# Kernel optimization log

Hardware: AMD Instinct MI355X
Metric: run time of the kernel (lower is better)

Reference implementation:

```python
import jax, jax.numpy as jnp
import numpy as np

N_HEAD = 16
NEG_INF = -1e9


def setup_inputs() -> dict:
    key = jax.random.key(0)
    k1, k2, k3 = jax.random.split(key, 3)
    B, S, D = 4, 1024, 1024
    x = jax.random.normal(k1, (B, S, D), dtype=jnp.float32)
    w_attn = jax.random.normal(k2, (D, 3 * D), dtype=jnp.float32) * 0.02
    b_attn = jnp.zeros((3 * D,), dtype=jnp.float32)
    w_proj = jax.random.normal(k3, (D, D), dtype=jnp.float32) * 0.02
    b_proj = jnp.zeros((D,), dtype=jnp.float32)
    return {"x": x, "w_attn": w_attn, "b_attn": b_attn,
            "w_proj": w_proj, "b_proj": b_proj}


def reference(x, w_attn, b_attn, w_proj, b_proj):
    B, S, D = x.shape
    H = N_HEAD
    hd = D // H
    # fused QKV Conv1D: addmm over flattened tokens
    qkv = x @ w_attn + b_attn                      # [B,S,3D]
    q, k, v = jnp.split(qkv, 3, axis=-1)           # each [B,S,D]
    # split heads -> [B,H,S,hd]
    def heads(t):
        return t.reshape(B, S, H, hd).transpose(0, 2, 1, 3)
    q, k, v = heads(q), heads(k), heads(v)
    # scaled dot-product with causal mask
    scores = jnp.einsum('bhqd,bhkd->bhqk', q, k) / jnp.sqrt(jnp.float32(hd))
    causal = jnp.tril(jnp.ones((S, S), dtype=bool))[None, None]  # [1,1,S,S]
    scores = jnp.where(causal, scores, NEG_INF)
    attn = jax.nn.softmax(scores, axis=-1)
    out = jnp.einsum('bhqk,bhkd->bhqd', attn, v)   # [B,H,S,hd]
    out = out.transpose(0, 2, 1, 3).reshape(B, S, D)  # merge heads
    # output projection Conv1D
    return out @ w_proj + b_proj
```

## Files before the change

### kernel.cpp

```cpp
#include <hip/hip_runtime.h>
#include <hip/hip_bf16.h>

typedef __attribute__((ext_vector_type(8))) __bf16 bf16x8;
typedef __attribute__((ext_vector_type(4))) float f32x4;

__device__ __forceinline__ unsigned short f2bf(float f) {
  unsigned int u = __builtin_bit_cast(unsigned int, f);
  u += 0x7fffu + ((u >> 16) & 1u);
  return (unsigned short)(u >> 16);
}

__device__ __forceinline__ unsigned int cvtpk_bf16(float a, float b) {
  unsigned int r;
  asm("v_cvt_pk_bf16_f32 %0, %1, %2" : "=v"(r) : "v"(a), "v"(b));
  return r;
}

__device__ __forceinline__ void gll16(const void* g, void* l) {
  __builtin_amdgcn_global_load_lds(
      (const __attribute__((address_space(1))) void*)g,
      (__attribute__((address_space(3))) void*)l, 16, 0, 0);
}

__device__ __forceinline__ bf16x8 lds_frag(const unsigned short* base, int row, int kbyte) {
  int off = row * 128 + (kbyte ^ ((row & 7) << 4));
  return *(const bf16x8*)((const char*)base + off);
}

__global__ __launch_bounds__(256) void prep(
    const float* __restrict__ x, unsigned short* __restrict__ xb,
    const float* __restrict__ wa, unsigned short* __restrict__ waT,
    const float* __restrict__ wp, unsigned short* __restrict__ wpT) {
  __shared__ float tile[32][33];
  const int b = blockIdx.x;
  const int t = threadIdx.x;
  if (b < 4096) {
    int i = (b * 256 + t) * 4;
    float4 v = *(const float4*)(x + i);
    ushort4 o;
    o.x = f2bf(v.x); o.y = f2bf(v.y); o.z = f2bf(v.z); o.w = f2bf(v.w);
    *(ushort4*)(xb + i) = o;
    return;
  }
  const float* in;
  unsigned short* out;
  int bid, N;
  if (b < 7168) { in = wa; out = waT; bid = b - 4096; N = 3072; }
  else          { in = wp; out = wpT; bid = b - 7168; N = 1024; }
  const int K = 1024;
  int nb = N >> 5;
  int bx = bid % nb, by = bid / nb;
  int n0 = bx << 5, k0 = by << 5;
  int c = t & 31, r0 = t >> 5;
#pragma unroll
  for (int i = 0; i < 4; ++i) {
    int r = r0 + i * 8;
    tile[r][c] = in[(size_t)(k0 + r) * N + n0 + c];
  }
  __syncthreads();
#pragma unroll
  for (int i = 0; i < 4; ++i) {
    int r = r0 + i * 8;
    out[(size_t)(n0 + r) * K + k0 + c] = f2bf(tile[c][r]);
  }
}

__global__ __launch_bounds__(512, 2) void gemm_qkv256(
    const unsigned short* __restrict__ A, const unsigned short* __restrict__ Bt,
    const float* __restrict__ bias,
    unsigned short* __restrict__ Qg, unsigned short* __restrict__ Kg,
    unsigned short* __restrict__ Vtg, int K) {
  __shared__ __align__(16) unsigned short SMEM[65536];
  unsigned short* const A0 = SMEM;
  unsigned short* const B0 = SMEM + 16384;
  unsigned short* const A1 = SMEM + 32768;
  unsigned short* const B1 = SMEM + 49152;
  const int t = threadIdx.x;
  const int l = t & 63, lr = l & 15, hi = l >> 4;
  const int w = t >> 6;
  const int wr = w >> 2, wc = w & 3;
  const int bid = (int)(blockIdx.x % 8) * 24 + (int)(blockIdx.x / 8);
  const int bm = bid / 12, bn = bid % 12;
  const int m0 = bm << 8, n0 = bn << 8;
  const int wbase = (t & ~63) * 8;

  f32x4 acc[8][4] = {};

  auto stage = [&](int kt, unsigned short* Ad, unsigned short* Bd) {
    const unsigned short* Ab = A + (size_t)m0 * K + kt * 64;
    const unsigned short* Bb = Bt + (size_t)n0 * K + kt * 64;
#pragma unroll
    for (int i = 0; i < 4; ++i) {
      int ci = i * 512 + t;
      int row = ci >> 3, cpos = ci & 7;
      int c = cpos ^ (row & 7);
      gll16(Ab + (size_t)row * K + c * 8, Ad + i * 4096 + wbase);
      gll16(Bb + (size_t)row * K + c * 8, Bd + i * 4096 + wbase);
    }
  };

  auto compute = [&](const unsigned short* Ad, const unsigned short* Bd) {
#pragma unroll
    for (int ks = 0; ks < 2; ++ks) {
      bf16x8 af[8], bv[4];
#pragma unroll
      for (int mi = 0; mi < 8; ++mi)
        af[mi] = lds_frag(Ad, wr * 128 + mi * 16 + lr, ks * 64 + hi * 16);
#pragma unroll
      for (int ni = 0; ni < 4; ++ni)
        bv[ni] = lds_frag(Bd, wc * 64 + ni * 16 + lr, ks * 64 + hi * 16);
      __builtin_amdgcn_s_setprio(1);
#pragma unroll
      for (int mi = 0; mi < 8; ++mi)
#pragma unroll
        for (int ni = 0; ni < 4; ++ni)
          acc[mi][ni] = __builtin_amdgcn_mfma_f32_16x16x32_bf16(af[mi], bv[ni], acc[mi][ni], 0, 0, 0);
      __builtin_amdgcn_s_setprio(0);
    }
  };

  const int nt = K >> 6;
  stage(0, A0, B0);
  __syncthreads();
  for (int T = 0; T < nt; ++T) {
    if (T + 1 < nt) stage(T + 1, (T & 1) ? A0 : A1, (T & 1) ? B0 : B1);
    compute((T & 1) ? A1 : A0, (T & 1) ? B1 : B0);
    __syncthreads();
  }

  if (n0 < 2048) {
    const float QSCALE = 0.125f * 1.4426950408889634f;
#pragma unroll
    for (int mi = 0; mi < 8; ++mi)
#pragma unroll
      for (int ni = 0; ni < 4; ++ni)
#pragma unroll
        for (int r = 0; r < 4; ++r) {
          int m = m0 + wr * 128 + mi * 16 + 4 * hi + r;
          int n = n0 + wc * 64 + ni * 16 + lr;
          float v = acc[mi][ni][r] + bias[n];
          int b = m >> 10, s = m & 1023;
          int d = n & 1023;
          int h = d >> 6, di = d & 63;
          int bh = (b << 4) + h;
          if (n < 1024) Qg[((size_t)(bh << 10) + s) * 64 + di] = f2bf(v * QSCALE);
          else          Kg[((size_t)(bh << 10) + s) * 64 + di] = f2bf(v);
        }
  } else {
    __syncthreads();
#pragma unroll
    for (int mi = 0; mi < 8; ++mi)
#pragma unroll
      for (int ni = 0; ni < 4; ++ni) {
        int nl = wc * 64 + ni * 16 + lr;
        int ml = wr * 128 + mi * 16 + 4 * hi;
        ushort4 pk;
        pk.x = f2bf(acc[mi][ni][0] + bias[n0 + nl]);
        pk.y = f2bf(acc[mi][ni][1] + bias[n0 + nl]);
        pk.z = f2bf(acc[mi][ni][2] + bias[n0 + nl]);
        pk.w = f2bf(acc[mi][ni][3] + bias[n0 + nl]);
        *(ushort4*)&SMEM[nl * 256 + (ml ^ ((nl & 7) << 3))] = pk;
      }
    __syncthreads();
    const int b = m0 >> 10;
    const int sbase = m0 & 1023;
#pragma unroll
    for (int it = 0; it < 16; ++it) {
      int nl = it * 16 + (t >> 5);
      int s0 = (t & 31) * 8;
      bf16x8 v8 = *(const bf16x8*)&SMEM[nl * 256 + (s0 ^ ((nl & 7) << 3))];
      int d = n0 - 2048 + nl;
      size_t row = ((size_t)((b << 4) + (d >> 6)) << 6) + (d & 63);
      *(bf16x8*)&Vtg[row * 1024 + sbase + s0] = v8;
    }
  }
}

__global__ __launch_bounds__(256, 2) void gemm_proj128(
    const unsigned short* __restrict__ A, const unsigned short* __restrict__ Bt,
    const float* __restrict__ bias, float* __restrict__ outf,
    int M, int N, int K) {
  __shared__ unsigned short A0[128 * 64], B0[128 * 64];
  __shared__ unsigned short A1[128 * 64], B1[128 * 64];
  const int t = threadIdx.x;
  const int w = t >> 6, l = t & 63, lr = l & 15, hi = l >> 4;
  const int wr = w >> 1, wc = w & 1;
  const int nbn = N >> 7;
  const int nwg = (M >> 7) * nbn;
  int bid = (int)blockIdx.x;
  if ((nwg & 7) == 0) bid = (bid % 8) * (nwg / 8) + bid / 8;
  const int bm = bid / nbn, bn = bid % nbn;
  const int m0 = bm << 7, n0 = bn << 7;
  const int wbase = (t & ~63) * 8;

  f32x4 acc[4][4] = {};

  auto stage = [&](int kt, unsigned short* Ad, unsigned short* Bd) {
    const unsigned short* Ab = A + (size_t)m0 * K + kt * 64;
    const unsigned short* Bb = Bt + (size_t)n0 * K + kt * 64;
#pragma unroll
    for (int i = 0; i < 4; ++i) {
      int ci = i * 256 + t;
      int row = ci >> 3, cpos = ci & 7;
      int c = cpos ^ (row & 7);
      gll16(Ab + (size_t)row * K + c * 8, Ad + i * 2048 + wbase);
      gll16(Bb + (size_t)row * K + c * 8, Bd + i * 2048 + wbase);
    }
  };

  auto compute = [&](const unsigned short* Ad, const unsigned short* Bd) {
#pragma unroll
    for (int ks = 0; ks < 2; ++ks) {
      bf16x8 af[4], bv[4];
#pragma unroll
      for (int mi = 0; mi < 4; ++mi)
        af[mi] = lds_frag(Ad, wr * 64 + mi * 16 + lr, ks * 64 + hi * 16);
#pragma unroll
      for (int ni = 0; ni < 4; ++ni)
        bv[ni] = lds_frag(Bd, wc * 64 + ni * 16 + lr, ks * 64 + hi * 16);
      __builtin_amdgcn_s_setprio(1);
#pragma unroll
      for (int mi = 0; mi < 4; ++mi)
#pragma unroll
        for (int ni = 0; ni < 4; ++ni)
          acc[mi][ni] = __builtin_amdgcn_mfma_f32_16x16x32_bf16(af[mi], bv[ni], acc[mi][ni], 0, 0, 0);
      __builtin_amdgcn_s_setprio(0);
    }
  };

  const int nt = K >> 6;
  stage(0, A0, B0);
  __syncthreads();
  for (int T = 0; T < nt; ++T) {
    if (T + 1 < nt) stage(T + 1, (T & 1) ? A0 : A1, (T & 1) ? B0 : B1);
    compute((T & 1) ? A1 : A0, (T & 1) ? B1 : B0);
    __syncthreads();
  }

#pragma unroll
  for (int mi = 0; mi < 4; ++mi)
#pragma unroll
    for (int ni = 0; ni < 4; ++ni)
#pragma unroll
      for (int r = 0; r < 4; ++r) {
        int m = m0 + wr * 64 + mi * 16 + 4 * hi + r;
        int n = n0 + wc * 64 + ni * 16 + lr;
        outf[(size_t)m * N + n] = acc[mi][ni][r] + bias[n];
      }
}

__global__ __launch_bounds__(256) void attn_kernel(
    const unsigned short* __restrict__ Qg, const unsigned short* __restrict__ Kg,
    const unsigned short* __restrict__ Vtg, unsigned short* __restrict__ Og) {
  __shared__ unsigned short K0[64 * 64], K1[64 * 64];
  __shared__ unsigned short Vb[64 * 64];
  __shared__ __align__(16) unsigned short Plds[4][16][72];
  const int bh = blockIdx.x & 63;
  const int qt = blockIdx.x >> 6;
  const int t = threadIdx.x;
  const int w = t >> 6, l = t & 63, lr = l & 15, hi = l >> 4;
  const unsigned short* Qbh = Qg + (size_t)bh * 65536;
  const unsigned short* Kbh = Kg + (size_t)bh * 65536;
  const unsigned short* Vbh = Vtg + (size_t)bh * 65536;
  const int q0 = qt * 64 + w * 16;
  const int wbase = (t & ~63) * 8;

  bf16x8 qf[2];
#pragma unroll
  for (int ks = 0; ks < 2; ++ks)
    qf[ks] = *(const bf16x8*)(Qbh + (size_t)(q0 + lr) * 64 + ks * 32 + hi * 8);

  f32x4 ocT[4] = {};
  float mrun = -1e30f, lrun = 0.f;
  const int thr = w * 16 + lr - 4 * hi;

  auto stageK = [&](int kt, unsigned short* Kd) {
#pragma unroll
    for (int i = 0; i < 2; ++i) {
      int ci = i * 256 + t;
      int row = ci >> 3, cpos = ci & 7;
      int c = cpos ^ (row & 7);
      gll16(Kbh + (size_t)(kt * 64 + row) * 64 + c * 8, Kd + i * 2048 + wbase);
    }
  };
  auto stageV = [&](int kt) {
#pragma unroll
    for (int i = 0; i < 2; ++i) {
      int ci = i * 256 + t;
      int row = ci >> 3, cpos = ci & 7;
      int c = cpos ^ (row & 7);
      gll16(Vbh + (size_t)row * 1024 + kt * 64 + c * 8, Vb + i * 2048 + wbase);
    }
  };

  stageK(0, K0);
  stageV(0);

  for (int kt = 0; kt <= qt; ++kt) {
    unsigned short* Kc = (kt & 1) ? K1 : K0;
    unsigned short* Kn = (kt & 1) ? K0 : K1;
    const bool pf = (kt < qt);

    asm volatile("s_waitcnt vmcnt(2)" ::: "memory");
    __builtin_amdgcn_s_barrier();

    if (pf) stageK(kt + 1, Kn);

    f32x4 sc[4] = {};
    __builtin_amdgcn_s_setprio(1);
#pragma unroll
    for (int c = 0; c < 4; ++c)
#pragma unroll
      for (int ks = 0; ks < 2; ++ks) {
        bf16x8 kf = lds_frag(Kc, c * 16 + lr, ks * 64 + hi * 16);
        sc[c] = __builtin_amdgcn_mfma_f32_16x16x32_bf16(kf, qf[ks], sc[c], 0, 0, 0);
      }
    __builtin_amdgcn_s_setprio(0);
    if (kt == qt) {
#pragma unroll
      for (int c = 0; c < 4; ++c)
#pragma unroll
        for (int r = 0; r < 4; ++r)
          if (c * 16 + r > thr) sc[c][r] = -1e30f;
    }

    float mx = sc[0][0];
#pragma unroll
    for (int c = 0; c < 4; ++c)
#pragma unroll
      for (int r = 0; r < 4; ++r) mx = fmaxf(mx, sc[c][r]);
    mx = fmaxf(mx, __shfl_xor(mx, 16));
    mx = fmaxf(mx, __shfl_xor(mx, 32));
    if (!__all(mx <= mrun)) {
      float mn = fmaxf(mrun, mx);
      float al = exp2f(mrun - mn);
      mrun = mn;
      lrun *= al;
#pragma unroll
      for (int c = 0; c < 4; ++c)
#pragma unroll
        for (int r = 0; r < 4; ++r) ocT[c][r] *= al;
    }
    float p[4][4], s = 0.f;
#pragma unroll
    for (int c = 0; c < 4; ++c)
#pragma unroll
      for (int r = 0; r < 4; ++r) {
        p[c][r] = exp2f(sc[c][r] - mrun);
        s += p[c][r];
      }
    s += __shfl_xor(s, 16);
    s += __shfl_xor(s, 32);
    lrun += s;

#pragma unroll
    for (int c = 0; c < 4; ++c) {
      uint2 pk;
      pk.x = cvtpk_bf16(p[c][0], p[c][1]);
      pk.y = cvtpk_bf16(p[c][2], p[c][3]);
      *(uint2*)&Plds[w][lr][c * 16 + 4 * hi] = pk;
    }
    asm volatile("s_waitcnt lgkmcnt(0)" ::: "memory");
    __builtin_amdgcn_sched_barrier(0);

    bf16x8 pb[2];
#pragma unroll
    for (int ks = 0; ks < 2; ++ks)
      pb[ks] = *(const bf16x8*)(&Plds[w][lr][ks * 32 + hi * 8]);

    if (pf) asm volatile("s_waitcnt vmcnt(2)" ::: "memory");
    else    asm volatile("s_waitcnt vmcnt(0)" ::: "memory");
    __builtin_amdgcn_s_barrier();

    __builtin_amdgcn_s_setprio(1);
#pragma unroll
    for (int c = 0; c < 4; ++c)
#pragma unroll
      for (int ks = 0; ks < 2; ++ks) {
        bf16x8 vf = lds_frag(Vb, c * 16 + lr, ks * 64 + hi * 16);
        ocT[c] = __builtin_amdgcn_mfma_f32_16x16x32_bf16(vf, pb[ks], ocT[c], 0, 0, 0);
      }
    __builtin_amdgcn_s_setprio(0);
    __builtin_amdgcn_s_barrier();
    if (pf) stageV(kt + 1);
  }

  const int b = bh >> 4, h = bh & 15;
  const float inv = 1.0f / lrun;
  const size_t rowbase = ((size_t)(b * 1024 + q0 + lr)) * 1024 + h * 64;
#pragma unroll
  for (int c = 0; c < 4; ++c) {
    uint2 o2;
    o2.x = cvtpk_bf16(ocT[c][0] * inv, ocT[c][1] * inv);
    o2.y = cvtpk_bf16(ocT[c][2] * inv, ocT[c][3] * inv);
    *(uint2*)&Og[rowbase + c * 16 + 4 * hi] = o2;
  }
}

extern "C" void kernel_launch(void* const* d_in, const int* in_sizes, int n_in,
                              void* d_out, int out_size, void* d_ws, size_t ws_size,
                              hipStream_t stream) {
  const float* x      = (const float*)d_in[0];
  const float* w_attn = (const float*)d_in[1];
  const float* b_attn = (const float*)d_in[2];
  const float* w_proj = (const float*)d_in[3];
  const float* b_proj = (const float*)d_in[4];
  float* out = (float*)d_out;

  unsigned short* ws  = (unsigned short*)d_ws;
  unsigned short* xb  = ws;
  unsigned short* waT = xb + 4096 * 1024;
  unsigned short* wpT = waT + 3072 * 1024;
  unsigned short* Qg  = wpT + 1024 * 1024;
  unsigned short* Kg  = Qg + 4194304;
  unsigned short* Vtg = Kg + 4194304;
  unsigned short* Og  = xb;

  prep<<<8192, 256, 0, stream>>>(x, xb, w_attn, waT, w_proj, wpT);
  gemm_qkv256<<<16 * 12, 512, 0, stream>>>(xb, waT, b_attn, Qg, Kg, Vtg, 1024);
  attn_kernel<<<1024, 256, 0, stream>>>(Qg, Kg, Vtg, Og);
  gemm_proj128<<<32 * 8, 256, 0, stream>>>(Og, wpT, b_proj, (float*)out, 4096, 1024, 1024);
}
```

Before: 97.59 us.

## Fuse x fp32-to-bf16 conversion into QKV GEMM A-tile loading

Removes the separate pass in prep that converts x to bf16. The QKV GEMM now reads fp32 x directly into registers, converts it to bf16 with packed cvt instructions, and writes it into the swizzled LDS tile after the compute step, keeping the double-buffer prefetch. This saves a full write and re-read of the 8 MB bf16 copy of x. In exchange, each GEMM block reads A as fp32 (twice the bytes, repeated across the 12 N-blocks), uses more registers for the prefetch, and loses the asynchronous global-to-LDS path for A.

Result: slower. 107.6 us (+10.3%).

```diff
diff --git a/kernel.cpp b/kernel.cpp
--- a/kernel.cpp
+++ b/kernel.cpp
@@ -28,25 +28,16 @@
 }
 
 __global__ __launch_bounds__(256) void prep(
-    const float* __restrict__ x, unsigned short* __restrict__ xb,
     const float* __restrict__ wa, unsigned short* __restrict__ waT,
     const float* __restrict__ wp, unsigned short* __restrict__ wpT) {
   __shared__ float tile[32][33];
   const int b = blockIdx.x;
   const int t = threadIdx.x;
-  if (b < 4096) {
-    int i = (b * 256 + t) * 4;
-    float4 v = *(const float4*)(x + i);
-    ushort4 o;
-    o.x = f2bf(v.x); o.y = f2bf(v.y); o.z = f2bf(v.z); o.w = f2bf(v.w);
-    *(ushort4*)(xb + i) = o;
-    return;
-  }
   const float* in;
   unsigned short* out;
   int bid, N;
-  if (b < 7168) { in = wa; out = waT; bid = b - 4096; N = 3072; }
-  else          { in = wp; out = wpT; bid = b - 7168; N = 1024; }
+  if (b < 3072) { in = wa; out = waT; bid = b; N = 3072; }
+  else          { in = wp; out = wpT; bid = b - 3072; N = 1024; }
   const int K = 1024;
   int nb = N >> 5;
   int bx = bid % nb, by = bid / nb;
@@ -66,7 +57,7 @@
 }
 
 __global__ __launch_bounds__(512, 2) void gemm_qkv256(
-    const unsigned short* __restrict__ A, const unsigned short* __restrict__ Bt,
+    const float* __restrict__ Xf, const unsigned short* __restrict__ Bt,
     const float* __restrict__ bias,
     unsigned short* __restrict__ Qg, unsigned short* __restrict__ Kg,
     unsigned short* __restrict__ Vtg, int K) {
@@ -85,16 +76,43 @@
   const int wbase = (t & ~63) * 8;
 
   f32x4 acc[8][4] = {};
-
-  auto stage = [&](int kt, unsigned short* Ad, unsigned short* Bd) {
-    const unsigned short* Ab = A + (size_t)m0 * K + kt * 64;
+  float4 fa[4][2];
+
+  size_t Aoff[4];
+#pragma unroll
+  for (int i = 0; i < 4; ++i) {
+    int ci = i * 512 + t;
+    int row = ci >> 3, cpos = ci & 7;
+    int c = cpos ^ (row & 7);
+    Aoff[i] = (size_t)(m0 + row) * 1024 + c * 8;
+  }
+
+  auto loadA = [&](int kt) {
+#pragma unroll
+    for (int i = 0; i < 4; ++i) {
+      const float* src = Xf + Aoff[i] + kt * 64;
+      fa[i][0] = *(const float4*)(src);
+      fa[i][1] = *(const float4*)(src + 4);
+    }
+  };
+  auto writeA = [&](unsigned short* Ad) {
+#pragma unroll
+    for (int i = 0; i < 4; ++i) {
+      uint4 pk;
+      pk.x = cvtpk_bf16(fa[i][0].x, fa[i][0].y);
+      pk.y = cvtpk_bf16(fa[i][0].z, fa[i][0].w);
+      pk.z = cvtpk_bf16(fa[i][1].x, fa[i][1].y);
+      pk.w = cvtpk_bf16(fa[i][1].z, fa[i][1].w);
+      *(uint4*)&Ad[(size_t)(i * 512 + t) * 8] = pk;
+    }
+  };
+  auto stageB = [&](int kt, unsigned short* Bd) {
     const unsigned short* Bb = Bt + (size_t)n0 * K + kt * 64;
 #pragma unroll
     for (int i = 0; i < 4; ++i) {
       int ci = i * 512 + t;
       int row = ci >> 3, cpos = ci & 7;
       int c = cpos ^ (row & 7);
-      gll16(Ab + (size_t)row * K + c * 8, Ad + i * 4096 + wbase);
       gll16(Bb + (size_t)row * K + c * 8, Bd + i * 4096 + wbase);
     }
   };
@@ -120,11 +138,17 @@
   };
 
   const int nt = K >> 6;
-  stage(0, A0, B0);
+  loadA(0);
+  stageB(0, B0);
+  writeA(A0);
   __syncthreads();
   for (int T = 0; T < nt; ++T) {
-    if (T + 1 < nt) stage(T + 1, (T & 1) ? A0 : A1, (T & 1) ? B0 : B1);
+    unsigned short* An = (T & 1) ? A0 : A1;
+    unsigned short* Bn = (T & 1) ? B0 : B1;
+    const bool pf = (T + 1 < nt);
+    if (pf) { loadA(T + 1); stageB(T + 1, Bn); }
     compute((T & 1) ? A1 : A0, (T & 1) ? B1 : B0);
+    if (pf) writeA(An);
     __syncthreads();
   }
 
@@ -408,16 +432,15 @@
   float* out = (float*)d_out;
 
   unsigned short* ws  = (unsigned short*)d_ws;
-  unsigned short* xb  = ws;
-  unsigned short* waT = xb + 4096 * 1024;
+  unsigned short* Og  = ws;
+  unsigned short* waT = Og + 4096 * 1024;
   unsigned short* wpT = waT + 3072 * 1024;
   unsigned short* Qg  = wpT + 1024 * 1024;
   unsigned short* Kg  = Qg + 4194304;
   unsigned short* Vtg = Kg + 4194304;
-  unsigned short* Og  = xb;
-
-  prep<<<8192, 256, 0, stream>>>(x, xb, w_attn, waT, w_proj, wpT);
-  gemm_qkv256<<<16 * 12, 512, 0, stream>>>(xb, waT, b_attn, Qg, Kg, Vtg, 1024);
+
+  prep<<<4096, 256, 0, stream>>>(w_attn, waT, w_proj, wpT);
+  gemm_qkv256<<<16 * 12, 512, 0, stream>>>(x, waT, b_attn, Qg, Kg, Vtg, 1024);
   attn_kernel<<<1024, 256, 0, stream>>>(Qg, Kg, Vtg, Og);
   gemm_proj128<<<32 * 8, 256, 0, stream>>>(Og, wpT, b_proj, (float*)out, 4096, 1024, 1024);
 }
```
